# Optimization experiments

Hardware: AMD Instinct MI355X
Metric: run time of the kernel (lower is better)

## Reference

```python
import jax, jax.numpy as jnp
import numpy as np

B, S, SM, D, H, DFF = 4, 1024, 1024, 1024, 16, 4096
HD = D // H
EPS = 1e-5


def _ln(x, g, b):
    mu = jnp.mean(x, axis=-1, keepdims=True)
    var = jnp.var(x, axis=-1, keepdims=True)
    return (x - mu) * jax.lax.rsqrt(var + EPS) * g + b


def setup_inputs() -> dict:
    key = jax.random.key(0)
    ks = jax.random.split(key, 20)
    w = lambda k, shp: (0.02 * jax.random.normal(k, shp, dtype=jnp.float32))
    return {
        "tgt": jax.random.normal(ks[0], (B, S, D), dtype=jnp.float32),
        "memory": jax.random.normal(ks[1], (B, SM, D), dtype=jnp.float32),
        # self-attn (no bias)
        "Wq": w(ks[2], (D, D)), "Wk": w(ks[3], (D, D)),
        "Wv": w(ks[4], (D, D)), "Wo": w(ks[5], (D, D)),
        # cross-attn nn.MultiheadAttention params
        "mha_in_w": w(ks[6], (3 * D, D)), "mha_in_b": jnp.zeros((3 * D,), jnp.float32),
        "mha_out_w": w(ks[7], (D, D)), "mha_out_b": jnp.zeros((D,), jnp.float32),
        # FFN
        "W1": w(ks[8], (DFF, D)), "b1": jnp.zeros((DFF,), jnp.float32),
        "W2": w(ks[9], (D, DFF)), "b2": jnp.zeros((D,), jnp.float32),
        # LayerNorms
        "g1": jnp.ones((D,), jnp.float32), "be1": jnp.zeros((D,), jnp.float32),
        "g2": jnp.ones((D,), jnp.float32), "be2": jnp.zeros((D,), jnp.float32),
        "g3": jnp.ones((D,), jnp.float32), "be3": jnp.zeros((D,), jnp.float32),
    }


def _self_attn(x, Wq, Wk, Wv, Wo):
    b, s, d = x.shape
    q = (x @ Wq.T).reshape(b, s, H, HD).transpose(0, 2, 1, 3)  # [B,H,S,hd]
    k = (x @ Wk.T).reshape(b, s, H, HD).transpose(0, 2, 1, 3)
    v = (x @ Wv.T).reshape(b, s, H, HD).transpose(0, 2, 1, 3)
    scores = jnp.einsum('bhqd,bhkd->bhqk', q, k) / jnp.sqrt(jnp.float32(HD))
    mask = jnp.triu(jnp.ones((s, s), dtype=bool), k=1)  # diagonal = full_S - S + 1 = 1
    scores = jnp.where(mask, -jnp.inf, scores)
    attn = jax.nn.softmax(scores, axis=-1)
    out = jnp.einsum('bhqk,bhkd->bhqd', attn, v).transpose(0, 2, 1, 3).reshape(b, s, d)
    return out @ Wo.T, k, v


def _cross_attn(q_in, kv_in, in_w, in_b, out_w, out_b):
    Wq, Wk, Wv = jnp.split(in_w, 3, axis=0)
    bq, bk, bv = jnp.split(in_b, 3, axis=0)
    b, s, d = q_in.shape
    sm = kv_in.shape[1]
    q = (q_in @ Wq.T + bq).reshape(b, s, H, HD).transpose(0, 2, 1, 3)
    k = (kv_in @ Wk.T + bk).reshape(b, sm, H, HD).transpose(0, 2, 1, 3)
    v = (kv_in @ Wv.T + bv).reshape(b, sm, H, HD).transpose(0, 2, 1, 3)
    scores = jnp.einsum('bhqd,bhkd->bhqk', q, k) / jnp.sqrt(jnp.float32(HD))
    attn = jax.nn.softmax(scores, axis=-1)
    out = jnp.einsum('bhqk,bhkd->bhqd', attn, v).transpose(0, 2, 1, 3).reshape(b, s, d)
    return out @ out_w.T + out_b


def reference(tgt, memory, Wq, Wk, Wv, Wo, mha_in_w, mha_in_b, mha_out_w, mha_out_b,
              W1, b1, W2, b2, g1, be1, g2, be2, g3, be3):
    # dropout = 0 (eval mode)
    sa_out, sa_k, sa_v = _self_attn(_ln(tgt, g1, be1), Wq, Wk, Wv, Wo)
    x = tgt + sa_out
    ca_out = _cross_attn(_ln(x, g2, be2), memory, mha_in_w, mha_in_b, mha_out_w, mha_out_b)
    x = x + ca_out
    ff = jax.nn.relu(_ln(x, g3, be3) @ W1.T + b1) @ W2.T + b2
    x = x + ff
    return x, sa_k, sa_v
```

## Files before the change

### kernel.cpp

```cpp
#include <hip/hip_runtime.h>

typedef __bf16 bf16_t;
typedef unsigned int u32;
typedef __attribute__((ext_vector_type(8))) __bf16 bf16x8;
typedef __attribute__((ext_vector_type(4))) __bf16 bf16x4;
typedef __attribute__((ext_vector_type(4))) float f32x4;


__device__ __forceinline__ bf16x8 load8f(const float* f) {
    float4 a = *(const float4*)f;
    float4 b = *(const float4*)(f + 4);
    bf16x8 r;
    r[0] = (bf16_t)a.x; r[1] = (bf16_t)a.y; r[2] = (bf16_t)a.z; r[3] = (bf16_t)a.w;
    r[4] = (bf16_t)b.x; r[5] = (bf16_t)b.y; r[6] = (bf16_t)b.z; r[7] = (bf16_t)b.w;
    return r;
}

__device__ __forceinline__ void gll16(const void* g, const void* l) {
    __builtin_amdgcn_global_load_lds(
        (const __attribute__((address_space(1))) u32*)(unsigned long long)g,
        (__attribute__((address_space(3))) u32*)(unsigned int)(unsigned long long)l,
        16, 0, 0);
}

__global__ __launch_bounds__(256) void conv_kernel(
    const float* __restrict__ Wq, const float* __restrict__ Wk,
    const float* __restrict__ Wv, const float* __restrict__ Wo,
    const float* __restrict__ Wio, const float* __restrict__ Woo,
    const float* __restrict__ W1, const float* __restrict__ W2,
    const float* __restrict__ mem, bf16_t* __restrict__ dst)
{
    long e = ((long)blockIdx.x * 256 + threadIdx.x) * 8;
    const float* s; long o;
    if      (e <  1048576) { s = Wq;  o = e; }
    else if (e <  2097152) { s = Wk;  o = e -  1048576; }
    else if (e <  3145728) { s = Wv;  o = e -  2097152; }
    else if (e <  4194304) { s = Wo;  o = e -  3145728; }
    else if (e <  7340032) { s = Wio; o = e -  4194304; }
    else if (e <  8388608) { s = Woo; o = e -  7340032; }
    else if (e < 12582912) { s = W1;  o = e -  8388608; }
    else if (e < 16777216) { s = W2;  o = e - 12582912; }
    else                   { s = mem; o = e - 16777216; }
    *(bf16x8*)&dst[e] = load8f(s + o);
}

__global__ __launch_bounds__(256) void ln_kernel(
    const float* __restrict__ x,
    const float* __restrict__ g, const float* __restrict__ be,
    bf16_t* __restrict__ out)
{
    int row = blockIdx.x, t = threadIdx.x;
    float4 q = *(const float4*)(x + (long)row * 1024 + t * 4);
    float v[4] = {q.x, q.y, q.z, q.w};
    float s = v[0] + v[1] + v[2] + v[3];
    float s2 = v[0]*v[0] + v[1]*v[1] + v[2]*v[2] + v[3]*v[3];
    for (int off = 32; off > 0; off >>= 1) {
        s  += __shfl_down(s, off);
        s2 += __shfl_down(s2, off);
    }
    __shared__ float rs[4], rq[4];
    int w = t >> 6;
    if ((t & 63) == 0) { rs[w] = s; rq[w] = s2; }
    __syncthreads();
    s  = rs[0] + rs[1] + rs[2] + rs[3];
    s2 = rq[0] + rq[1] + rq[2] + rq[3];
    float mean = s * (1.0f / 1024.0f);
    float var  = s2 * (1.0f / 1024.0f) - mean * mean;
    float rstd = rsqrtf(var + 1e-5f);
    int c = t * 4;
    for (int i = 0; i < 4; i++)
        out[(long)row * 1024 + c + i] =
            (bf16_t)((v[i] - mean) * rstd * g[c + i] + be[c + i]);
}

__global__ __launch_bounds__(512, 2) void gemm_big(
    const bf16_t* __restrict__ A, int lda,
    const bf16_t* __restrict__ Wb, long w_off, int ldw, int K,
    const float* __restrict__ bias, long b_off,
    const float* resid,
    void* o0, void* o1, void* o2, int mode, int N, int do_relu,
    void* o3, void* o4)
{
    __shared__ __align__(16) bf16_t As[2][256 * 64];
    __shared__ __align__(16) bf16_t Bs[2][256 * 64];
    int tid = threadIdx.x;
    int lin = blockIdx.y * gridDim.x + blockIdx.x;
    int mb = lin % gridDim.y, nb = lin / gridDim.y;
    int m0 = mb << 8, n0 = nb << 8;
    int w = tid >> 6, lane = tid & 63;
    int l15 = lane & 15, quad = lane >> 4;
    int wm = w >> 2, wn = w & 3;
    int srow = lane >> 3;
    int cgo  = ((lane & 7) ^ srow) << 3;

    const bf16_t* Wg = Wb + w_off;
    int nk = K >> 6;

    f32x4 acc[8][4];
    #pragma unroll
    for (int i = 0; i < 8; i++)
        #pragma unroll
        for (int j = 0; j < 4; j++)
            acc[i][j] = (f32x4){0.f, 0.f, 0.f, 0.f};

#define STAGEB(P, KK)                                                         \
    _Pragma("unroll")                                                         \
    for (int g = 0; g < 4; g++) {                                             \
        int rg = ((g << 3) + w) << 3;                                         \
        gll16(A  + (long)(m0 + rg + srow) * lda + (KK) + cgo, &As[P][rg << 6]); \
        gll16(Wg + (long)(n0 + rg + srow) * ldw + (KK) + cgo, &Bs[P][rg << 6]); \
    }

    STAGEB(0, 0)
    asm volatile("s_waitcnt vmcnt(0)");
    __builtin_amdgcn_s_barrier();
    __builtin_amdgcn_sched_barrier(0);

    for (int t = 0; t < nk; t++) {
        int p = t & 1;
        bf16x8 bfr[4][2];
        #pragma unroll
        for (int q = 0; q < 4; q++) {
            bf16x8 af[2][2];
            #pragma unroll
            for (int i2 = 0; i2 < 2; i2++)
                #pragma unroll
                for (int ks = 0; ks < 2; ks++) {
                    int row = (wm << 7) + (((q << 1) + i2) << 4) + l15;
                    int sl = ((quad + (ks << 2)) ^ (l15 & 7)) << 3;
                    af[i2][ks] = *(const bf16x8*)&As[p][(row << 6) + sl];
                }
            if (q == 0) {
                #pragma unroll
                for (int j = 0; j < 4; j++)
                    #pragma unroll
                    for (int ks = 0; ks < 2; ks++) {
                        int row = (wn << 6) + (j << 4) + l15;
                        int sl = ((quad + (ks << 2)) ^ (l15 & 7)) << 3;
                        bfr[j][ks] = *(const bf16x8*)&Bs[p][(row << 6) + sl];
                    }
                if (t + 1 < nk) STAGEB(p ^ 1, (t + 1) << 6)
            }
            asm volatile("s_waitcnt lgkmcnt(0)");
            __builtin_amdgcn_sched_barrier(0);
            __builtin_amdgcn_s_setprio(1);
            #pragma unroll
            for (int i2 = 0; i2 < 2; i2++)
                #pragma unroll
                for (int j = 0; j < 4; j++)
                    #pragma unroll
                    for (int ks = 0; ks < 2; ks++)
                        acc[(q << 1) + i2][j] = __builtin_amdgcn_mfma_f32_16x16x32_bf16(
                            af[i2][ks], bfr[j][ks], acc[(q << 1) + i2][j], 0, 0, 0);
            __builtin_amdgcn_s_setprio(0);
            __builtin_amdgcn_sched_barrier(0);
        }
        if (t + 1 < nk) { asm volatile("s_waitcnt vmcnt(0)"); }
        __builtin_amdgcn_s_barrier();
        __builtin_amdgcn_sched_barrier(0);
    }
#undef STAGEB

    int rb = quad << 2;
    for (int i = 0; i < 8; i++) {
        for (int j = 0; j < 4; j++) {
            int col = n0 + (wn << 6) + (j << 4) + l15;
            float bv = bias ? bias[b_off + col] : 0.0f;
            for (int r = 0; r < 4; r++) {
                int row = m0 + (wm << 7) + (i << 4) + rb + r;
                float v = acc[i][j][r] + bv;
                if (do_relu) v = fmaxf(v, 0.0f);
                if (mode == 0) {
                    long idx = (long)row * N + col;
                    if (resid) v += resid[idx];
                    if (o0) ((float*)o0)[idx] = v;
                    if (o1) ((bf16_t*)o1)[idx] = (bf16_t)v;
                    if (o2) {
                        long hidx = (((long)(row >> 10) * 16 + (col >> 6)) * 1024
                                     + (row & 1023)) * 64 + (col & 63);
                        ((bf16_t*)o2)[hidx] = (bf16_t)v;
                    }
                } else {
                    int seg = col >> 10, c = col & 1023;
                    long hidx = (((long)(row >> 10) * 16 + (c >> 6)) * 1024
                                 + (row & 1023)) * 64 + (c & 63);
                    if (mode == 1) {
                        if (seg == 0)      ((bf16_t*)o0)[hidx] = (bf16_t)v;
                        else if (seg == 1) {
                            ((float*)o1)[hidx] = v;
                            if (o3) ((bf16_t*)o3)[hidx] = (bf16_t)v;
                        } else {
                            ((float*)o2)[hidx] = v;
                            if (o4) ((bf16_t*)o4)[hidx] = (bf16_t)v;
                        }
                    } else {
                        if (seg == 0)      ((bf16_t*)o0)[hidx] = (bf16_t)v;
                        else               ((bf16_t*)o1)[hidx] = (bf16_t)v;
                    }
                }
            }
        }
    }
}

template<int NJ>
__global__ __launch_bounds__(256) void gemm_fast(
    const bf16_t* __restrict__ A, int lda, int a_head,
    const bf16_t* __restrict__ Wb, long w_off, int ldw, int K,
    const float* __restrict__ bias, long b_off,
    const float* resid,
    void* o0, void* o1, void* o2, int mode, int N, int do_relu,
    void* o3, void* o4)
{
    constexpr int BN = NJ << 5;
    __shared__ __align__(16) bf16_t As[2][128 * 64];
    __shared__ __align__(16) bf16_t Bs[2][BN * 64];
    int tid = threadIdx.x;
    int lin = blockIdx.y * gridDim.x + blockIdx.x;
    int mb = lin % gridDim.y, nb = lin / gridDim.y;
    int m0 = mb << 7, n0 = nb * BN;
    int w = tid >> 6, lane = tid & 63;
    int l15 = lane & 15, quad = lane >> 4;
    int wr = (w >> 1) << 6, wc = (w & 1) * (BN >> 1);

    int srow = lane >> 3;
    int cgo  = ((lane & 7) ^ srow) << 3;

    f32x4 acc[4][NJ];
    for (int i = 0; i < 4; i++)
        for (int j = 0; j < NJ; j++)
            acc[i][j] = (f32x4){0.f, 0.f, 0.f, 0.f};

    const bf16_t* Wg = Wb + w_off;
    int nk = K >> 6;

#define STAGE(P, KK)                                                          \
    {                                                                         \
        const bf16_t* Ab; long astr;                                          \
        if (a_head) {                                                         \
            int hh = (KK) >> 6;                                               \
            Ab = A + ((((long)(m0 >> 10)) * 16 + hh) * 1024 + (m0 & 1023)) * 64; \
            astr = 64;                                                        \
        } else {                                                              \
            Ab = A + (long)m0 * lda + (KK);                                   \
            astr = lda;                                                       \
        }                                                                     \
        const bf16_t* Bb = Wg + (long)n0 * ldw + (KK);                        \
        for (int t = 0; t < 4; t++) {                                         \
            int rb2 = (w << 5) + (t << 3);                                    \
            gll16(Ab + (long)(rb2 + srow) * astr + cgo, &As[P][rb2 << 6]);    \
        }                                                                     \
        for (int t = 0; t < NJ; t++) {                                        \
            int rb2 = w * (BN >> 2) + (t << 3);                               \
            gll16(Bb + (long)(rb2 + srow) * ldw + cgo, &Bs[P][rb2 << 6]);     \
        }                                                                     \
    }

#define COMPUTE(P)                                                            \
    for (int ks = 0; ks < 2; ks++) {                                          \
        bf16x8 af[4], bf_[NJ];                                                \
        int gA = quad + (ks << 2);                                            \
        int sl = (gA ^ (l15 & 7)) << 3;                                       \
        for (int i = 0; i < 4; i++)                                           \
            af[i]  = *(const bf16x8*)&As[P][((wr + (i << 4) + l15) << 6) + sl]; \
        for (int j = 0; j < NJ; j++)                                          \
            bf_[j] = *(const bf16x8*)&Bs[P][((wc + (j << 4) + l15) << 6) + sl]; \
        for (int i = 0; i < 4; i++)                                           \
            for (int j = 0; j < NJ; j++)                                      \
                acc[i][j] = __builtin_amdgcn_mfma_f32_16x16x32_bf16(          \
                    af[i], bf_[j], acc[i][j], 0, 0, 0);                       \
    }

    STAGE(0, 0)
    __syncthreads();
    int p = 0;
    for (int kt = 0; kt < nk; kt++) {
        if (kt + 1 < nk) STAGE(p ^ 1, (kt + 1) << 6)
        COMPUTE(p)
        __syncthreads();
        p ^= 1;
    }
#undef STAGE
#undef COMPUTE

    int rb = quad << 2;
    for (int i = 0; i < 4; i++) {
        for (int j = 0; j < NJ; j++) {
            int col = n0 + wc + (j << 4) + l15;
            float bv = bias ? bias[b_off + col] : 0.0f;
            for (int r = 0; r < 4; r++) {
                int row = m0 + wr + (i << 4) + rb + r;
                float v = acc[i][j][r] + bv;
                if (do_relu) v = fmaxf(v, 0.0f);
                if (mode == 0) {
                    long idx = (long)row * N + col;
                    if (resid) v += resid[idx];
                    if (o0) ((float*)o0)[idx] = v;
                    if (o1) ((bf16_t*)o1)[idx] = (bf16_t)v;
                    if (o2) {
                        long hidx = (((long)(row >> 10) * 16 + (col >> 6)) * 1024
                                     + (row & 1023)) * 64 + (col & 63);
                        ((bf16_t*)o2)[hidx] = (bf16_t)v;
                    }
                } else {
                    int seg = col >> 10, c = col & 1023;
                    long hidx = (((long)(row >> 10) * 16 + (c >> 6)) * 1024
                                 + (row & 1023)) * 64 + (c & 63);
                    if (mode == 1) {
                        if (seg == 0)      ((bf16_t*)o0)[hidx] = (bf16_t)v;
                        else if (seg == 1) {
                            ((float*)o1)[hidx] = v;
                            if (o3) ((bf16_t*)o3)[hidx] = (bf16_t)v;
                        } else {
                            ((float*)o2)[hidx] = v;
                            if (o4) ((bf16_t*)o4)[hidx] = (bf16_t)v;
                        }
                    } else {
                        if (seg == 0)      ((bf16_t*)o0)[hidx] = (bf16_t)v;
                        else               ((bf16_t*)o1)[hidx] = (bf16_t)v;
                    }
                }
            }
        }
    }
}

#define LDT 40

__global__ __launch_bounds__(256) void gemm_nt(
    const void* __restrict__ A, int lda, int a_head, int a_f32,
    const float* __restrict__ W, long w_off, int ldw,
    int K,
    const float* __restrict__ bias, long b_off,
    const float* __restrict__ resid,
    float*  out_f32, bf16_t* __restrict__ out_b16,
    float*  __restrict__ out_hf32, bf16_t* __restrict__ out_hb16,
    int N, int do_relu)
{
    __shared__ bf16_t As[128 * LDT];
    __shared__ bf16_t Bs[128 * LDT];
    int tid = threadIdx.x;
    int m0 = blockIdx.y << 7, n0 = blockIdx.x << 7;
    int wave = tid >> 6, lane = tid & 63;
    int wr = (wave >> 1) << 6;
    int wc = (wave & 1) << 6;
    int l15 = lane & 15, quad = lane >> 4;

    f32x4 acc[4][4];
    for (int i = 0; i < 4; i++)
        for (int j = 0; j < 4; j++)
            acc[i][j] = (f32x4){0.f, 0.f, 0.f, 0.f};

    int sr = tid >> 2;
    int sc = (tid & 3) << 3;

    for (int k0 = 0; k0 < K; k0 += 32) {
        int kk = k0 + sc;
        long ia0, ia1;
        if (a_head) {
            int hh = kk >> 6, dd = kk & 63;
            int r0g = m0 + sr, r1g = r0g + 64;
            ia0 = ((((long)(r0g >> 10) * 16 + hh) * 1024 + (r0g & 1023)) << 6) + dd;
            ia1 = ((((long)(r1g >> 10) * 16 + hh) * 1024 + (r1g & 1023)) << 6) + dd;
        } else {
            ia0 = (long)(m0 + sr) * lda + kk;
            ia1 = (long)(m0 + sr + 64) * lda + kk;
        }
        long iw0 = w_off + (long)(n0 + sr) * ldw + kk;
        long iw1 = w_off + (long)(n0 + sr + 64) * ldw + kk;
        __syncthreads();
        if (a_f32) {
            *(bf16x8*)&As[sr * LDT + sc]        = load8f((const float*)A + ia0);
            *(bf16x8*)&As[(sr + 64) * LDT + sc] = load8f((const float*)A + ia1);
        } else {
            *(bf16x8*)&As[sr * LDT + sc]        = *(const bf16x8*)((const bf16_t*)A + ia0);
            *(bf16x8*)&As[(sr + 64) * LDT + sc] = *(const bf16x8*)((const bf16_t*)A + ia1);
        }
        *(bf16x8*)&Bs[sr * LDT + sc]        = load8f(W + iw0);
        *(bf16x8*)&Bs[(sr + 64) * LDT + sc] = load8f(W + iw1);
        __syncthreads();
        bf16x8 afr[4], bfr[4];
        for (int i = 0; i < 4; i++)
            afr[i] = *(const bf16x8*)&As[(wr + i * 16 + l15) * LDT + quad * 8];
        for (int j = 0; j < 4; j++)
            bfr[j] = *(const bf16x8*)&Bs[(wc + j * 16 + l15) * LDT + quad * 8];
        for (int i = 0; i < 4; i++)
            for (int j = 0; j < 4; j++)
                acc[i][j] = __builtin_amdgcn_mfma_f32_16x16x32_bf16(
                    afr[i], bfr[j], acc[i][j], 0, 0, 0);
    }

    int rb = quad << 2;
    for (int i = 0; i < 4; i++) {
        for (int j = 0; j < 4; j++) {
            int col = n0 + wc + (j << 4) + l15;
            float bv = bias ? bias[b_off + col] : 0.0f;
            for (int r = 0; r < 4; r++) {
                int row = m0 + wr + (i << 4) + rb + r;
                float v = acc[i][j][r] + bv;
                if (do_relu) v = fmaxf(v, 0.0f);
                long idx = (long)row * N + col;
                if (resid) v += resid[idx];
                if (out_f32) out_f32[idx] = v;
                if (out_b16) out_b16[idx] = (bf16_t)v;
                if (out_hf32 || out_hb16) {
                    int bb = row >> 10, ss = row & 1023, hh = col >> 6, dd = col & 63;
                    long hidx = (((long)bb * 16 + hh) * 1024 + ss) * 64 + dd;
                    if (out_hf32) out_hf32[hidx] = v;
                    if (out_hb16) out_hb16[hidx] = (bf16_t)v;
                }
            }
        }
    }
}

__global__ __launch_bounds__(256) void attn_kernel(
    const bf16_t* __restrict__ Q, const void* __restrict__ K,
    const void* __restrict__ V, bf16_t* __restrict__ AO,
    int Sk, int causal, int kv_f32)
{
    __shared__ __align__(16) bf16_t Qs[64 * 72];
    __shared__ __align__(16) bf16_t Ks[64 * 72];
    __shared__ __align__(16) bf16_t Vt[64 * 72];
    __shared__ __align__(16) bf16_t Ps[64 * 72];

    int tid = threadIdx.x;
    int qt = blockIdx.x, bh = blockIdx.y;
    int w = tid >> 6, lane = tid & 63;
    int l15 = lane & 15, quad = lane >> 4;
    int wr = w << 4;
    int rowq = wr + (quad << 2);

    {
        int r = tid >> 2, c16 = (tid & 3) << 4;
        const bf16_t* Qb = Q + ((long)bh * 1024 + qt * 64) * 64;
        bf16x8 a = *(const bf16x8*)&Qb[r * 64 + c16];
        bf16x8 b = *(const bf16x8*)&Qb[r * 64 + c16 + 8];
        *(bf16x8*)&Qs[r * 72 + c16] = a;
        *(bf16x8*)&Qs[r * 72 + c16 + 8] = b;
    }

    float m_i[4] = {-1e30f, -1e30f, -1e30f, -1e30f};
    float l_i[4] = {0.f, 0.f, 0.f, 0.f};
    f32x4 o_acc[4];
    for (int j = 0; j < 4; j++) o_acc[j] = (f32x4){0.f, 0.f, 0.f, 0.f};

    int nt = causal ? (qt + 1) : (Sk >> 6);
    long kvbase = (long)bh * Sk * 64;

    for (int kt = 0; kt < nt; kt++) {
        __syncthreads();
        {
            int r = tid >> 2, c16 = (tid & 3) << 4;
            long off = kvbase + (long)((kt << 6) + r) * 64 + c16;
            bf16x8 k0, k1, v0, v1;
            if (kv_f32) {
                const float* kp = (const float*)K + off;
                const float* vp = (const float*)V + off;
                k0 = load8f(kp); k1 = load8f(kp + 8);
                v0 = load8f(vp); v1 = load8f(vp + 8);
            } else {
                k0 = *(const bf16x8*)((const bf16_t*)K + off);
                k1 = *(const bf16x8*)((const bf16_t*)K + off + 8);
                v0 = *(const bf16x8*)((const bf16_t*)V + off);
                v1 = *(const bf16x8*)((const bf16_t*)V + off + 8);
            }
            *(bf16x8*)&Ks[r * 72 + c16] = k0;
            *(bf16x8*)&Ks[r * 72 + c16 + 8] = k1;
            for (int i = 0; i < 8; i++) {
                Vt[(c16 + i) * 72 + r]     = v0[i];
                Vt[(c16 + 8 + i) * 72 + r] = v1[i];
            }
        }
        __syncthreads();

        f32x4 s[4];
        for (int j = 0; j < 4; j++) s[j] = (f32x4){0.f, 0.f, 0.f, 0.f};
        for (int ks = 0; ks < 2; ks++) {
            int sl = (quad + (ks << 2)) << 3;
            bf16x8 aq = *(const bf16x8*)&Qs[(wr + l15) * 72 + sl];
            for (int j = 0; j < 4; j++) {
                bf16x8 bk = *(const bf16x8*)&Ks[((j << 4) + l15) * 72 + sl];
                s[j] = __builtin_amdgcn_mfma_f32_16x16x32_bf16(aq, bk, s[j], 0, 0, 0);
            }
        }

        int diag = causal && (kt == qt);
        for (int rr = 0; rr < 4; rr++) {
            float sv[4];
            for (int j = 0; j < 4; j++) {
                float x = s[j][rr] * 0.125f;
                if (diag && ((j << 4) + l15 > rowq + rr)) x = -1e30f;
                sv[j] = x;
            }
            float mx = fmaxf(fmaxf(sv[0], sv[1]), fmaxf(sv[2], sv[3]));
            for (int off = 1; off < 16; off <<= 1) mx = fmaxf(mx, __shfl_xor(mx, off));
            float mnew = fmaxf(m_i[rr], mx);
            float alpha = __expf(m_i[rr] - mnew);
            float p0 = __expf(sv[0] - mnew), p1 = __expf(sv[1] - mnew);
            float p2 = __expf(sv[2] - mnew), p3 = __expf(sv[3] - mnew);
            float rsum = p0 + p1 + p2 + p3;
            for (int off = 1; off < 16; off <<= 1) rsum += __shfl_xor(rsum, off);
            m_i[rr] = mnew;
            l_i[rr] = l_i[rr] * alpha + rsum;
            for (int j = 0; j < 4; j++) o_acc[j][rr] *= alpha;
            bf16_t* pr = &Ps[(rowq + rr) * 72 + l15];
            pr[0]  = (bf16_t)p0; pr[16] = (bf16_t)p1;
            pr[32] = (bf16_t)p2; pr[48] = (bf16_t)p3;
        }
        __syncthreads();

        for (int ks = 0; ks < 2; ks++) {
            int sl = (quad + (ks << 2)) << 3;
            bf16x8 ap = *(const bf16x8*)&Ps[(wr + l15) * 72 + sl];
            for (int j = 0; j < 4; j++) {
                bf16x8 bv = *(const bf16x8*)&Vt[((j << 4) + l15) * 72 + sl];
                o_acc[j] = __builtin_amdgcn_mfma_f32_16x16x32_bf16(ap, bv, o_acc[j], 0, 0, 0);
            }
        }
    }

    bf16_t* Ob = AO + ((long)bh * 1024 + qt * 64) * 64;
    for (int rr = 0; rr < 4; rr++) {
        float inv = 1.0f / l_i[rr];
        for (int j = 0; j < 4; j++)
            Ob[(rowq + rr) * 64 + (j << 4) + l15] = (bf16_t)(o_acc[j][rr] * inv);
    }
}

extern "C" void kernel_launch(void* const* d_in, const int* in_sizes, int n_in,
                              void* d_out, int out_size, void* d_ws, size_t ws_size,
                              hipStream_t stream)
{
    (void)in_sizes; (void)n_in; (void)out_size;
    const float* tgt       = (const float*)d_in[0];
    const float* mem       = (const float*)d_in[1];
    const float* Wq        = (const float*)d_in[2];
    const float* Wk        = (const float*)d_in[3];
    const float* Wv        = (const float*)d_in[4];
    const float* Wo        = (const float*)d_in[5];
    const float* mha_in_w  = (const float*)d_in[6];
    const float* mha_in_b  = (const float*)d_in[7];
    const float* mha_out_w = (const float*)d_in[8];
    const float* mha_out_b = (const float*)d_in[9];
    const float* W1        = (const float*)d_in[10];
    const float* b1        = (const float*)d_in[11];
    const float* W2        = (const float*)d_in[12];
    const float* b2        = (const float*)d_in[13];
    const float* g1        = (const float*)d_in[14];
    const float* be1       = (const float*)d_in[15];
    const float* g2        = (const float*)d_in[16];
    const float* be2       = (const float*)d_in[17];
    const float* g3        = (const float*)d_in[18];
    const float* be3       = (const float*)d_in[19];

    float* out_x = (float*)d_out;
    float* out_k = out_x + (1 << 22);
    float* out_v = out_k + (1 << 22);

    bf16_t* R0 = (bf16_t*)d_ws;
    bf16_t* R1 = R0 + (1 << 22);
    bf16_t* R2 = R1 + (1 << 22);

    dim3 blk(256);
    dim3 blk5(512);
    dim3 gA(16, 64);

    if (ws_size >= ((size_t)96 << 20)) {
        bf16_t* Hff  = R2 + (1 << 22);
        bf16_t* Wb   = (bf16_t*)((char*)d_ws + ((size_t)56 << 20));
        bf16_t* memb = Wb + 16777216;
        bf16_t* saKb = Hff;
        bf16_t* saVb = Hff + (1 << 22);
        const long WO_OFF  = 3145728;
        const long CQ_OFF  = 4194304;
        const long CKV_OFF = 5242880;
        const long CO_OFF  = 7340032;
        const long W1_OFF  = 8388608;
        const long W2_OFF  = 12582912;

        conv_kernel<<<10240, blk, 0, stream>>>(Wq, Wk, Wv, Wo, mha_in_w,
                                               mha_out_w, W1, W2, mem, Wb);

        ln_kernel<<<4096, blk, 0, stream>>>(tgt, g1, be1, R0);
        gemm_big<<<dim3(12, 16), blk5, 0, stream>>>(R0, 1024, Wb, 0, 1024, 1024,
                                                    nullptr, 0, nullptr,
                                                    R1, out_k, out_v, 1, 3072, 0,
                                                    saKb, saVb);
        attn_kernel<<<gA, blk, 0, stream>>>(R1, saKb, saVb, R1, 1024, 1, 0);
        gemm_fast<2><<<dim3(16, 32), blk, 0, stream>>>(R1, 0, 1, Wb, WO_OFF, 1024, 1024,
                                                       nullptr, 0, tgt,
                                                       out_x, nullptr, nullptr, 0, 1024, 0,
                                                       nullptr, nullptr);

        ln_kernel<<<4096, blk, 0, stream>>>(out_x, g2, be2, R0);
        gemm_fast<2><<<dim3(16, 32), blk, 0, stream>>>(R0, 1024, 0, Wb, CQ_OFF, 1024, 1024,
                                                       mha_in_b, 0, nullptr,
                                                       nullptr, nullptr, R1, 0, 1024, 0,
                                                       nullptr, nullptr);
        gemm_big<<<dim3(8, 16), blk5, 0, stream>>>(memb, 1024, Wb, CKV_OFF, 1024, 1024,
                                                   mha_in_b, 1024, nullptr,
                                                   R2, R0, nullptr, 2, 2048, 0,
                                                   nullptr, nullptr);
        attn_kernel<<<gA, blk, 0, stream>>>(R1, R2, R0, R1, 1024, 0, 0);
        gemm_fast<2><<<dim3(16, 32), blk, 0, stream>>>(R1, 0, 1, Wb, CO_OFF, 1024, 1024,
                                                       mha_out_b, 0, out_x,
                                                       out_x, nullptr, nullptr, 0, 1024, 0,
                                                       nullptr, nullptr);

        ln_kernel<<<4096, blk, 0, stream>>>(out_x, g3, be3, R0);
        gemm_big<<<dim3(16, 16), blk5, 0, stream>>>(R0, 1024, Wb, W1_OFF, 1024, 1024,
                                                    b1, 0, nullptr,
                                                    nullptr, Hff, nullptr, 0, 4096, 1,
                                                    nullptr, nullptr);
        gemm_fast<2><<<dim3(16, 32), blk, 0, stream>>>(Hff, 4096, 0, Wb, W2_OFF, 4096, 4096,
                                                       b2, 0, out_x,
                                                       out_x, nullptr, nullptr, 0, 1024, 0,
                                                       nullptr, nullptr);
        return;
    }

    dim3 gD(8, 32);
    dim3 gF1(32, 16);
    dim3 gF2(8, 16);

    ln_kernel<<<4096, blk, 0, stream>>>(tgt, g1, be1, R0);
    gemm_nt<<<gD, blk, 0, stream>>>(R0, 1024, 0, 0, Wq, 0, 1024, 1024,
                                    nullptr, 0, nullptr, nullptr, nullptr,
                                    nullptr, R1, 1024, 0);
    gemm_nt<<<gD, blk, 0, stream>>>(R0, 1024, 0, 0, Wk, 0, 1024, 1024,
                                    nullptr, 0, nullptr, nullptr, nullptr,
                                    out_k, nullptr, 1024, 0);
    gemm_nt<<<gD, blk, 0, stream>>>(R0, 1024, 0, 0, Wv, 0, 1024, 1024,
                                    nullptr, 0, nullptr, nullptr, nullptr,
                                    out_v, nullptr, 1024, 0);
    attn_kernel<<<gA, blk, 0, stream>>>(R1, out_k, out_v, R1, 1024, 1, 1);
    gemm_nt<<<gD, blk, 0, stream>>>(R1, 0, 1, 0, Wo, 0, 1024, 1024,
                                    nullptr, 0, tgt, out_x, nullptr,
                                    nullptr, nullptr, 1024, 0);

    ln_kernel<<<4096, blk, 0, stream>>>(out_x, g2, be2, R0);
    gemm_nt<<<gD, blk, 0, stream>>>(R0, 1024, 0, 0, mha_in_w, 0, 1024, 1024,
                                    mha_in_b, 0, nullptr, nullptr, nullptr,
                                    nullptr, R1, 1024, 0);
    gemm_nt<<<gD, blk, 0, stream>>>(mem, 1024, 0, 1, mha_in_w, (long)1 << 20, 1024, 1024,
                                    mha_in_b, 1024, nullptr, nullptr, nullptr,
                                    nullptr, R2, 1024, 0);
    gemm_nt<<<gD, blk, 0, stream>>>(mem, 1024, 0, 1, mha_in_w, (long)2 << 20, 1024, 1024,
                                    mha_in_b, 2048, nullptr, nullptr, nullptr,
                                    nullptr, R0, 1024, 0);
    attn_kernel<<<gA, blk, 0, stream>>>(R1, R2, R0, R1, 1024, 0, 0);
    gemm_nt<<<gD, blk, 0, stream>>>(R1, 0, 1, 0, mha_out_w, 0, 1024, 1024,
                                    mha_out_b, 0, out_x, out_x, nullptr,
                                    nullptr, nullptr, 1024, 0);

    ln_kernel<<<4096, blk, 0, stream>>>(out_x, g3, be3, R0);
    for (int c = 0; c < 2; c++) {
        const bf16_t* Ac = R0 + (long)c * 2048 * 1024;
        bf16_t*       Hc = R1;
        float*        Xc = out_x + (long)c * 2048 * 1024;
        gemm_nt<<<gF1, blk, 0, stream>>>(Ac, 1024, 0, 0, W1, 0, 1024, 1024,
                                         b1, 0, nullptr, nullptr, Hc,
                                         nullptr, nullptr, 4096, 1);
        gemm_nt<<<gF2, blk, 0, stream>>>(Hc, 4096, 0, 0, W2, 0, 4096, 4096,
                                         b2, 0, Xc, Xc, nullptr,
                                         nullptr, nullptr, 1024, 0);
    }
}
```

Before: 676.7 us.

## Add MFMA flash-attention kernel with transposed V and templated GEMM tile height

Adds attn_fast, a flash-attention style kernel that computes QK^T and PV with bf16 MFMA using an online softmax. It reads V in a pre-transposed [head, dim, seq] layout, which the GEMM epilogue now writes as packed bf16x4 stores. gemm_big gains an M-tile template parameter, and the cross-attention KV projection uses a 128-row tile so it launches twice as many blocks. The risk is that the existing attn_kernel consumers are replaced, and correctness depends on the new V layout matching what attn_fast expects.

Result: faster. 623.4 us (-7.9%).

```diff
diff --git a/kernel.cpp b/kernel.cpp
--- a/kernel.cpp
+++ b/kernel.cpp
@@ -73,6 +73,7 @@
             (bf16_t)((v[i] - mean) * rstd * g[c + i] + be[c + i]);
 }
 
+template<int MI>
 __global__ __launch_bounds__(512, 2) void gemm_big(
     const bf16_t* __restrict__ A, int lda,
     const bf16_t* __restrict__ Wb, long w_off, int ldw, int K,
@@ -81,12 +82,13 @@
     void* o0, void* o1, void* o2, int mode, int N, int do_relu,
     void* o3, void* o4)
 {
-    __shared__ __align__(16) bf16_t As[2][256 * 64];
+    constexpr int BM = MI << 5;
+    __shared__ __align__(16) bf16_t As[2][BM * 64];
     __shared__ __align__(16) bf16_t Bs[2][256 * 64];
     int tid = threadIdx.x;
     int lin = blockIdx.y * gridDim.x + blockIdx.x;
     int mb = lin % gridDim.y, nb = lin / gridDim.y;
-    int m0 = mb << 8, n0 = nb << 8;
+    int m0 = mb * BM, n0 = nb << 8;
     int w = tid >> 6, lane = tid & 63;
     int l15 = lane & 15, quad = lane >> 4;
     int wm = w >> 2, wn = w & 3;
@@ -96,18 +98,22 @@
     const bf16_t* Wg = Wb + w_off;
     int nk = K >> 6;
 
-    f32x4 acc[8][4];
+    f32x4 acc[MI][4];
     #pragma unroll
-    for (int i = 0; i < 8; i++)
+    for (int i = 0; i < MI; i++)
         #pragma unroll
         for (int j = 0; j < 4; j++)
             acc[i][j] = (f32x4){0.f, 0.f, 0.f, 0.f};
 
 #define STAGEB(P, KK)                                                         \
     _Pragma("unroll")                                                         \
+    for (int g = 0; g < (MI >> 1); g++) {                                     \
+        int rg = ((g << 3) + w) << 3;                                         \
+        gll16(A  + (long)(m0 + rg + srow) * lda + (KK) + cgo, &As[P][rg << 6]); \
+    }                                                                         \
+    _Pragma("unroll")                                                         \
     for (int g = 0; g < 4; g++) {                                             \
         int rg = ((g << 3) + w) << 3;                                         \
-        gll16(A  + (long)(m0 + rg + srow) * lda + (KK) + cgo, &As[P][rg << 6]); \
         gll16(Wg + (long)(n0 + rg + srow) * ldw + (KK) + cgo, &Bs[P][rg << 6]); \
     }
 
@@ -120,13 +126,13 @@
         int p = t & 1;
         bf16x8 bfr[4][2];
         #pragma unroll
-        for (int q = 0; q < 4; q++) {
+        for (int q = 0; q < (MI >> 1); q++) {
             bf16x8 af[2][2];
             #pragma unroll
             for (int i2 = 0; i2 < 2; i2++)
                 #pragma unroll
                 for (int ks = 0; ks < 2; ks++) {
-                    int row = (wm << 7) + (((q << 1) + i2) << 4) + l15;
+                    int row = wm * (MI << 4) + (((q << 1) + i2) << 4) + l15;
                     int sl = ((quad + (ks << 2)) ^ (l15 & 7)) << 3;
                     af[i2][ks] = *(const bf16x8*)&As[p][(row << 6) + sl];
                 }
@@ -162,16 +168,22 @@
 #undef STAGEB
 
     int rb = quad << 2;
-    for (int i = 0; i < 8; i++) {
+    for (int i = 0; i < MI; i++) {
         for (int j = 0; j < 4; j++) {
             int col = n0 + (wn << 6) + (j << 4) + l15;
             float bv = bias ? bias[b_off + col] : 0.0f;
+            int row0 = m0 + wm * (MI << 4) + (i << 4) + rb;
+            float vv[4];
             for (int r = 0; r < 4; r++) {
-                int row = m0 + (wm << 7) + (i << 4) + rb + r;
                 float v = acc[i][j][r] + bv;
                 if (do_relu) v = fmaxf(v, 0.0f);
-                if (mode == 0) {
+                vv[r] = v;
+            }
+            if (mode == 0) {
+                for (int r = 0; r < 4; r++) {
+                    int row = row0 + r;
                     long idx = (long)row * N + col;
+                    float v = vv[r];
                     if (resid) v += resid[idx];
                     if (o0) ((float*)o0)[idx] = v;
                     if (o1) ((bf16_t*)o1)[idx] = (bf16_t)v;
@@ -180,22 +192,39 @@
                                      + (row & 1023)) * 64 + (col & 63);
                         ((bf16_t*)o2)[hidx] = (bf16_t)v;
                     }
-                } else {
-                    int seg = col >> 10, c = col & 1023;
-                    long hidx = (((long)(row >> 10) * 16 + (c >> 6)) * 1024
-                                 + (row & 1023)) * 64 + (c & 63);
-                    if (mode == 1) {
-                        if (seg == 0)      ((bf16_t*)o0)[hidx] = (bf16_t)v;
-                        else if (seg == 1) {
-                            ((float*)o1)[hidx] = v;
-                            if (o3) ((bf16_t*)o3)[hidx] = (bf16_t)v;
-                        } else {
-                            ((float*)o2)[hidx] = v;
-                            if (o4) ((bf16_t*)o4)[hidx] = (bf16_t)v;
+                }
+            } else {
+                int seg = col >> 10, c = col & 1023;
+                long hb = (long)(row0 >> 10) * 16 + (c >> 6);
+                long hidx0 = (hb * 1024 + (row0 & 1023)) * 64 + (c & 63);
+                if (mode == 1) {
+                    if (seg == 0) {
+                        for (int r = 0; r < 4; r++)
+                            ((bf16_t*)o0)[hidx0 + r * 64] = (bf16_t)vv[r];
+                    } else if (seg == 1) {
+                        for (int r = 0; r < 4; r++) {
+                            ((float*)o1)[hidx0 + r * 64] = vv[r];
+                            if (o3) ((bf16_t*)o3)[hidx0 + r * 64] = (bf16_t)vv[r];
                         }
                     } else {
-                        if (seg == 0)      ((bf16_t*)o0)[hidx] = (bf16_t)v;
-                        else               ((bf16_t*)o1)[hidx] = (bf16_t)v;
+                        for (int r = 0; r < 4; r++)
+                            ((float*)o2)[hidx0 + r * 64] = vv[r];
+                        if (o4) {
+                            long vt0 = (hb * 64 + (c & 63)) * 1024 + (row0 & 1023);
+                            bf16x4 pk;
+                            for (int r = 0; r < 4; r++) pk[r] = (bf16_t)vv[r];
+                            *(bf16x4*)&((bf16_t*)o4)[vt0] = pk;
+                        }
+                    }
+                } else {
+                    if (seg == 0) {
+                        for (int r = 0; r < 4; r++)
+                            ((bf16_t*)o0)[hidx0 + r * 64] = (bf16_t)vv[r];
+                    } else {
+                        long vt0 = (hb * 64 + (c & 63)) * 1024 + (row0 & 1023);
+                        bf16x4 pk;
+                        for (int r = 0; r < 4; r++) pk[r] = (bf16_t)vv[r];
+                        *(bf16x4*)&((bf16_t*)o1)[vt0] = pk;
                     }
                 }
             }
@@ -414,6 +443,112 @@
     }
 }
 
+__global__ __launch_bounds__(256) void attn_fast(
+    const bf16_t* __restrict__ Q, const bf16_t* __restrict__ K,
+    const bf16_t* __restrict__ V, bf16_t* __restrict__ AO,
+    int Sk, int causal)
+{
+    __shared__ __align__(16) bf16_t Ks[64 * 72];
+    __shared__ __align__(16) bf16_t Vt[64 * 72];
+    __shared__ __align__(16) bf16_t Ps[64 * 72];
+
+    int tid = threadIdx.x;
+    int qt = blockIdx.x, bh = blockIdx.y;
+    int w = tid >> 6, lane = tid & 63;
+    int l15 = lane & 15, quad = lane >> 4;
+    int wr = w << 4;
+    int rowq = wr + (quad << 2);
+
+    const bf16_t* Qb = Q + ((long)bh * 1024 + (qt << 6)) * 64;
+    bf16x8 aq0 = *(const bf16x8*)&Qb[(wr + l15) * 64 + (quad << 3)];
+    bf16x8 aq1 = *(const bf16x8*)&Qb[(wr + l15) * 64 + (quad << 3) + 32];
+
+    float m_i[4] = {-1e30f, -1e30f, -1e30f, -1e30f};
+    float l_i[4] = {0.f, 0.f, 0.f, 0.f};
+    f32x4 o_acc[4];
+    for (int j = 0; j < 4; j++) o_acc[j] = (f32x4){0.f, 0.f, 0.f, 0.f};
+
+    int nt = causal ? (qt + 1) : (Sk >> 6);
+    long kb = (long)bh * Sk * 64;
+    long vb = (long)bh * 64 * Sk;
+
+    int r = tid >> 2, c16 = (tid & 3) << 4;
+
+    bf16x8 kr0, kr1, vr0, vr1;
+    {
+        const bf16_t* kp = K + kb + (long)r * 64 + c16;
+        const bf16_t* vp = V + vb + (long)r * Sk + c16;
+        kr0 = *(const bf16x8*)kp;       kr1 = *(const bf16x8*)(kp + 8);
+        vr0 = *(const bf16x8*)vp;       vr1 = *(const bf16x8*)(vp + 8);
+    }
+
+    for (int kt = 0; kt < nt; kt++) {
+        __syncthreads();
+        *(bf16x8*)&Ks[r * 72 + c16]     = kr0;
+        *(bf16x8*)&Ks[r * 72 + c16 + 8] = kr1;
+        *(bf16x8*)&Vt[r * 72 + c16]     = vr0;
+        *(bf16x8*)&Vt[r * 72 + c16 + 8] = vr1;
+        if (kt + 1 < nt) {
+            const bf16_t* kp = K + kb + (((long)(kt + 1) << 6) + r) * 64 + c16;
+            const bf16_t* vp = V + vb + (long)r * Sk + ((kt + 1) << 6) + c16;
+            kr0 = *(const bf16x8*)kp;   kr1 = *(const bf16x8*)(kp + 8);
+            vr0 = *(const bf16x8*)vp;   vr1 = *(const bf16x8*)(vp + 8);
+        }
+        __syncthreads();
+
+        f32x4 s[4];
+        for (int j = 0; j < 4; j++) s[j] = (f32x4){0.f, 0.f, 0.f, 0.f};
+        for (int j = 0; j < 4; j++) {
+            bf16x8 bk0 = *(const bf16x8*)&Ks[((j << 4) + l15) * 72 + (quad << 3)];
+            bf16x8 bk1 = *(const bf16x8*)&Ks[((j << 4) + l15) * 72 + (quad << 3) + 32];
+            s[j] = __builtin_amdgcn_mfma_f32_16x16x32_bf16(aq0, bk0, s[j], 0, 0, 0);
+            s[j] = __builtin_amdgcn_mfma_f32_16x16x32_bf16(aq1, bk1, s[j], 0, 0, 0);
+        }
+
+        int diag = causal && (kt == qt);
+        for (int rr = 0; rr < 4; rr++) {
+            float sv[4];
+            for (int j = 0; j < 4; j++) {
+                float x = s[j][rr] * 0.125f;
+                if (diag && ((j << 4) + l15 > rowq + rr)) x = -1e30f;
+                sv[j] = x;
+            }
+            float mx = fmaxf(fmaxf(sv[0], sv[1]), fmaxf(sv[2], sv[3]));
+            for (int off = 1; off < 16; off <<= 1) mx = fmaxf(mx, __shfl_xor(mx, off));
+            float mnew = fmaxf(m_i[rr], mx);
+            float alpha = __expf(m_i[rr] - mnew);
+            float p0 = __expf(sv[0] - mnew), p1 = __expf(sv[1] - mnew);
+            float p2 = __expf(sv[2] - mnew), p3 = __expf(sv[3] - mnew);
+            float rsum = p0 + p1 + p2 + p3;
+            for (int off = 1; off < 16; off <<= 1) rsum += __shfl_xor(rsum, off);
+            m_i[rr] = mnew;
+            l_i[rr] = l_i[rr] * alpha + rsum;
+            for (int j = 0; j < 4; j++) o_acc[j][rr] *= alpha;
+            bf16_t* pr = &Ps[(rowq + rr) * 72 + l15];
+            pr[0]  = (bf16_t)p0; pr[16] = (bf16_t)p1;
+            pr[32] = (bf16_t)p2; pr[48] = (bf16_t)p3;
+        }
+        asm volatile("s_waitcnt lgkmcnt(0)" ::: "memory");
+        __builtin_amdgcn_sched_barrier(0);
+
+        for (int ks = 0; ks < 2; ks++) {
+            int sl = (quad + (ks << 2)) << 3;
+            bf16x8 ap = *(const bf16x8*)&Ps[(wr + l15) * 72 + sl];
+            for (int j = 0; j < 4; j++) {
+                bf16x8 bv = *(const bf16x8*)&Vt[((j << 4) + l15) * 72 + sl];
+                o_acc[j] = __builtin_amdgcn_mfma_f32_16x16x32_bf16(ap, bv, o_acc[j], 0, 0, 0);
+            }
+        }
+    }
+
+    bf16_t* Ob = AO + ((long)bh * 1024 + (qt << 6)) * 64;
+    for (int rr = 0; rr < 4; rr++) {
+        float inv = 1.0f / l_i[rr];
+        for (int j = 0; j < 4; j++)
+            Ob[(rowq + rr) * 64 + (j << 4) + l15] = (bf16_t)(o_acc[j][rr] * inv);
+    }
+}
+
 __global__ __launch_bounds__(256) void attn_kernel(
     const bf16_t* __restrict__ Q, const void* __restrict__ K,
     const void* __restrict__ V, bf16_t* __restrict__ AO,
@@ -583,11 +718,11 @@
                                                mha_out_w, W1, W2, mem, Wb);
 
         ln_kernel<<<4096, blk, 0, stream>>>(tgt, g1, be1, R0);
-        gemm_big<<<dim3(12, 16), blk5, 0, stream>>>(R0, 1024, Wb, 0, 1024, 1024,
-                                                    nullptr, 0, nullptr,
-                                                    R1, out_k, out_v, 1, 3072, 0,
-                                                    saKb, saVb);
-        attn_kernel<<<gA, blk, 0, stream>>>(R1, saKb, saVb, R1, 1024, 1, 0);
+        gemm_big<8><<<dim3(12, 16), blk5, 0, stream>>>(R0, 1024, Wb, 0, 1024, 1024,
+                                                       nullptr, 0, nullptr,
+                                                       R1, out_k, out_v, 1, 3072, 0,
+                                                       saKb, saVb);
+        attn_fast<<<gA, blk, 0, stream>>>(R1, saKb, saVb, R1, 1024, 1);
         gemm_fast<2><<<dim3(16, 32), blk, 0, stream>>>(R1, 0, 1, Wb, WO_OFF, 1024, 1024,
                                                        nullptr, 0, tgt,
                                                        out_x, nullptr, nullptr, 0, 1024, 0,
@@ -598,21 +733,21 @@
                                                        mha_in_b, 0, nullptr,
                                                        nullptr, nullptr, R1, 0, 1024, 0,
                                                        nullptr, nullptr);
-        gemm_big<<<dim3(8, 16), blk5, 0, stream>>>(memb, 1024, Wb, CKV_OFF, 1024, 1024,
-                                                   mha_in_b, 1024, nullptr,
-                                                   R2, R0, nullptr, 2, 2048, 0,
-                                                   nullptr, nullptr);
-        attn_kernel<<<gA, blk, 0, stream>>>(R1, R2, R0, R1, 1024, 0, 0);
+        gemm_big<4><<<dim3(8, 32), blk5, 0, stream>>>(memb, 1024, Wb, CKV_OFF, 1024, 1024,
+                                                      mha_in_b, 1024, nullptr,
+                                                      R2, R0, nullptr, 2, 2048, 0,
+                                                      nullptr, nullptr);
+        attn_fast<<<gA, blk, 0, stream>>>(R1, R2, R0, R1, 1024, 0);
         gemm_fast<2><<<dim3(16, 32), blk, 0, stream>>>(R1, 0, 1, Wb, CO_OFF, 1024, 1024,
                                                        mha_out_b, 0, out_x,
                                                        out_x, nullptr, nullptr, 0, 1024, 0,
                                                        nullptr, nullptr);
 
         ln_kernel<<<4096, blk, 0, stream>>>(out_x, g3, be3, R0);
-        gemm_big<<<dim3(16, 16), blk5, 0, stream>>>(R0, 1024, Wb, W1_OFF, 1024, 1024,
-                                                    b1, 0, nullptr,
-                                                    nullptr, Hff, nullptr, 0, 4096, 1,
-                                                    nullptr, nullptr);
+        gemm_big<8><<<dim3(16, 16), blk5, 0, stream>>>(R0, 1024, Wb, W1_OFF, 1024, 1024,
+                                                       b1, 0, nullptr,
+                                                       nullptr, Hff, nullptr, 0, 4096, 1,
+                                                       nullptr, nullptr);
         gemm_fast<2><<<dim3(16, 32), blk, 0, stream>>>(Hff, 4096, 0, Wb, W2_OFF, 4096, 4096,
                                                        b2, 0, out_x,
                                                        out_x, nullptr, nullptr, 0, 1024, 0,
```
